# Kernel tuning notes

Hardware: AMD Instinct MI355X
Metric: run time of the kernel (lower is better)

Reference implementation:

```python
import jax, jax.numpy as jnp
import numpy as np

KH, KW = 3, 3
PAD = 1
IN_C = 3
OUT_C = 16
QUBITS = 5            # max(ceil(log2(3*3*3))=5, ceil(log2(16))=4)
QDEPTH = 1
DIM = 2 ** QUBITS     # 32 amplitudes per patch
FEAT = KH * KW * IN_C # 27 unfolded features per patch
EPS = 0.001           # self.almost_zero


def setup_inputs() -> dict:
    key = jax.random.key(0)
    k1, k2 = jax.random.split(key)
    x = jax.random.normal(k1, (8, 3, 224, 224), dtype=jnp.float32)
    # StronglyEntanglingLayer rotation angles (depth, qubits, 3) in [0, 2pi)
    weights = jax.random.uniform(k2, (QDEPTH, QUBITS, 3), dtype=jnp.float32,
                                 minval=0.0, maxval=2.0 * np.pi)
    return {"x": x, "weights": weights}


def _rot(phi, theta, omega):
    # PennyLane/qandle Rot(phi, theta, omega) = RZ(omega) RY(theta) RZ(phi)
    c = jnp.cos(theta * 0.5).astype(jnp.complex64)
    s = jnp.sin(theta * 0.5).astype(jnp.complex64)
    em = jnp.exp(-0.5j * (phi + omega))   # e^{-i(phi+omega)/2}
    ep = jnp.exp(0.5j * (phi + omega))
    epm = jnp.exp(0.5j * (phi - omega))
    emp = jnp.exp(-0.5j * (phi - omega))
    row0 = jnp.stack([em * c, -epm * s])
    row1 = jnp.stack([emp * s, ep * c])
    return jnp.stack([row0, row1])  # (2, 2) complex64


def _apply_1q(psi, U, q):
    # psi: (N, 2, 2, 2, 2, 2); apply 2x2 unitary on qubit q
    psi = jnp.moveaxis(psi, 1 + q, -1)
    psi = psi @ U.T  # new_a = sum_b U[a,b] psi[..., b]
    return jnp.moveaxis(psi, -1, 1 + q)


def _cnot(psi, c, t):
    # control qubit c, target qubit t: flip target where control == 1
    p0, p1 = jnp.split(psi, 2, axis=1 + c)
    p1 = jnp.flip(p1, axis=1 + t)
    return jnp.concatenate([p0, p1], axis=1 + c)


def reference(x, weights):
    b, cin, h, w = x.shape
    # --- Unfold (kernel 3x3, pad 1, stride 1) -> (b, c*kh*kw, h*w), torch layout ---
    xp = jnp.pad(x, ((0, 0), (0, 0), (PAD, PAD), (PAD, PAD)))
    cols = jnp.stack([xp[:, :, i:i + h, j:j + w]
                      for i in range(KH) for j in range(KW)], axis=2)  # (b, c, 9, h, w)
    v = cols.reshape(b, FEAT, h * w)
    # rearrange 'batch channel feat -> (batch feat) channel'
    v = jnp.transpose(v, (0, 2, 1)).reshape(b * h * w, FEAT) + EPS
    # --- AmplitudeEmbedding: pad with 0 to 2^qubits, L2-normalize ---
    v = jnp.pad(v, ((0, 0), (0, DIM - FEAT)))
    psi = (v / jnp.linalg.norm(v, axis=1, keepdims=True)).astype(jnp.complex64)
    psi = psi.reshape((b * h * w,) + (2,) * QUBITS)
    # --- StronglyEntanglingLayer: Rot on each qubit, then CNOT ring ---
    for d in range(QDEPTH):
        for q in range(QUBITS):
            U = _rot(weights[d, q, 0], weights[d, q, 1], weights[d, q, 2])
            psi = _apply_1q(psi, U, q)
        for q in range(QUBITS):
            psi = _cnot(psi, q, (q + 1) % QUBITS)
    # --- MeasureJointProbability: |amplitude|^2 over all basis states ---
    psi = psi.reshape(b * h * w, DIM)
    probs = psi.real ** 2 + psi.imag ** 2
    # --- post-process: keep first out_channels, scale ---
    out = probs[:, :OUT_C] * (OUT_C / 2.0)
    # rearrange '(batch h w) channel -> batch channel h w'
    out = jnp.transpose(out.reshape(b, h * w, OUT_C), (0, 2, 1))
    return out.reshape(b, OUT_C, h, w)
```

## Files before the change

### kernel.cpp

```cpp
#include <hip/hip_runtime.h>

#define H 224
#define W 224
#define NB 8
#define OUTC 16
#define FEAT 27
#define EPSV 0.001f

__global__ void build_M(const float* __restrict__ w, float2* __restrict__ M) {
    __shared__ float sre[32][33];
    __shared__ float sim_[32][33];
    const int j = threadIdx.x;

    for (int i = 0; i < 32; ++i) {
        sre[j][i] = (i == j) ? 1.0f : 0.0f;
        sim_[j][i] = 0.0f;
    }

    for (int q = 0; q < 5; ++q) {
        float phi = w[q * 3 + 0];
        float th  = w[q * 3 + 1];
        float om  = w[q * 3 + 2];
        float ch = cosf(0.5f * th), sh = sinf(0.5f * th);
        float al = 0.5f * (phi + om), be = 0.5f * (phi - om);
        float ca = cosf(al), sa = sinf(al);
        float cb = cosf(be), sb = sinf(be);
        float u00r =  ca * ch, u00i = -sa * ch;
        float u01r = -cb * sh, u01i = -sb * sh;
        float u10r =  cb * sh, u10i = -sb * sh;
        float u11r =  ca * ch, u11i =  sa * ch;

        int m = 1 << (4 - q);
        for (int i = 0; i < 32; ++i) {
            if (i & m) continue;
            float a0r = sre[j][i],     a0i = sim_[j][i];
            float a1r = sre[j][i | m], a1i = sim_[j][i | m];
            sre[j][i]     = u00r * a0r - u00i * a0i + u01r * a1r - u01i * a1i;
            sim_[j][i]    = u00r * a0i + u00i * a0r + u01r * a1i + u01i * a1r;
            sre[j][i | m] = u10r * a0r - u10i * a0i + u11r * a1r - u11i * a1i;
            sim_[j][i | m]= u10r * a0i + u10i * a0r + u11r * a1i + u11i * a1r;
        }
    }

    for (int q = 0; q < 5; ++q) {
        int mc = 1 << (4 - q);
        int mt = 1 << (4 - ((q + 1) % 5));
        for (int i = 0; i < 32; ++i) {
            if ((i & mc) && !(i & mt)) {
                int i2 = i | mt;
                float tr = sre[j][i]; sre[j][i] = sre[j][i2]; sre[j][i2] = tr;
                float ti = sim_[j][i]; sim_[j][i] = sim_[j][i2]; sim_[j][i2] = ti;
            }
        }
    }

    if (j < FEAT) {
        for (int k = 0; k < OUTC; ++k) {
            M[k * FEAT + j] = make_float2(sre[j][k], sim_[j][k]);
        }
    }
}

__global__ __launch_bounds__(256) void qconv_main(const float* __restrict__ x,
                                                  const float2* __restrict__ M,
                                                  float* __restrict__ out) {
    int p = blockIdx.x * 256 + threadIdx.x;
    int xx = p % W;
    int rest = p / W;
    int yy = rest % H;
    int b = rest / H;

    const float* xb = x + b * (3 * H * W);

    float v[FEAT];
    #pragma unroll
    for (int c = 0; c < 3; ++c) {
        #pragma unroll
        for (int ki = 0; ki < 3; ++ki) {
            #pragma unroll
            for (int kj = 0; kj < 3; ++kj) {
                int iy = yy + ki - 1;
                int ix = xx + kj - 1;
                float val = 0.0f;
                if (iy >= 0 && iy < H && ix >= 0 && ix < W)
                    val = xb[c * (H * W) + iy * W + ix];
                v[c * 9 + ki * 3 + kj] = val + EPSV;
            }
        }
    }

    float n2 = 0.0f;
    #pragma unroll
    for (int f = 0; f < FEAT; ++f) n2 = fmaf(v[f], v[f], n2);
    float scale = 8.0f / n2;

    float* ob = out + b * (OUTC * H * W) + yy * W + xx;
    #pragma unroll
    for (int k = 0; k < OUTC; ++k) {
        float re = 0.0f, im = 0.0f;
        #pragma unroll
        for (int f = 0; f < FEAT; ++f) {
            float2 m = M[k * FEAT + f];
            re = fmaf(m.x, v[f], re);
            im = fmaf(m.y, v[f], im);
        }
        ob[k * (H * W)] = (re * re + im * im) * scale;
    }
}

extern "C" void kernel_launch(void* const* d_in, const int* in_sizes, int n_in,
                              void* d_out, int out_size, void* d_ws, size_t ws_size,
                              hipStream_t stream) {
    const float* x = (const float*)d_in[0];
    const float* w = (const float*)d_in[1];
    float* out = (float*)d_out;
    float2* M = (float2*)d_ws;

    build_M<<<1, 32, 0, stream>>>(w, M);

    int pixels = out_size / OUTC;
    int blocks = (pixels + 255) / 256;
    qconv_main<<<blocks, 256, 0, stream>>>(x, M, out);
}
```

Baseline: 96.27 us.

## Pre-pad input with eps, compute 4 pixels per thread with vector loads

A prep kernel now writes a zero-padded, eps-added copy of the input into a workspace buffer, and the same launch builds the matrix M in its last block. The main kernel stages M in shared memory, and each thread handles 4 horizontally adjacent pixels and 8 of the 16 output channels. It loads 3x6 windows per channel with float4/float2 loads and stores outputs as float4. This is meant to cut redundant neighbourhood loads, remove bounds checks, and raise work per thread, at the cost of an extra full pass writing and reading a padded copy of the input.

```diff
diff --git a/kernel.cpp b/kernel.cpp
--- a/kernel.cpp
+++ b/kernel.cpp
@@ -2,109 +2,153 @@
 
 #define H 224
 #define W 224
-#define NB 8
+#define HW (H * W)
 #define OUTC 16
 #define FEAT 27
 #define EPSV 0.001f
+#define PH 226
+#define PW 228
+#define PLANE (PH * PW)
+#define NPAD (24 * PLANE)
+#define PAD_BLOCKS ((NPAD + 255) / 256)
 
-__global__ void build_M(const float* __restrict__ w, float2* __restrict__ M) {
-    __shared__ float sre[32][33];
-    __shared__ float sim_[32][33];
-    const int j = threadIdx.x;
+typedef float f4 __attribute__((ext_vector_type(4)));
+typedef float f2 __attribute__((ext_vector_type(2)));
 
-    for (int i = 0; i < 32; ++i) {
-        sre[j][i] = (i == j) ? 1.0f : 0.0f;
-        sim_[j][i] = 0.0f;
+__global__ __launch_bounds__(256) void prep(const float* __restrict__ x,
+                                            const float* __restrict__ w,
+                                            float* __restrict__ pbuf,
+                                            float2* __restrict__ M) {
+    if (blockIdx.x == gridDim.x - 1) {
+        __shared__ float sre[32][33];
+        __shared__ float sim_[32][33];
+        const int j = threadIdx.x;
+        if (j >= 32) return;
+
+        for (int i = 0; i < 32; ++i) {
+            sre[j][i] = (i == j) ? 1.0f : 0.0f;
+            sim_[j][i] = 0.0f;
+        }
+        for (int q = 0; q < 5; ++q) {
+            float phi = w[q * 3 + 0];
+            float th  = w[q * 3 + 1];
+            float om  = w[q * 3 + 2];
+            float ch = cosf(0.5f * th), sh = sinf(0.5f * th);
+            float al = 0.5f * (phi + om), be = 0.5f * (phi - om);
+            float ca = cosf(al), sa = sinf(al);
+            float cb = cosf(be), sb = sinf(be);
+            float u00r =  ca * ch, u00i = -sa * ch;
+            float u01r = -cb * sh, u01i = -sb * sh;
+            float u10r =  cb * sh, u10i = -sb * sh;
+            float u11r =  ca * ch, u11i =  sa * ch;
+            int m = 1 << (4 - q);
+            for (int i = 0; i < 32; ++i) {
+                if (i & m) continue;
+                float a0r = sre[j][i],     a0i = sim_[j][i];
+                float a1r = sre[j][i | m], a1i = sim_[j][i | m];
+                sre[j][i]      = u00r * a0r - u00i * a0i + u01r * a1r - u01i * a1i;
+                sim_[j][i]     = u00r * a0i + u00i * a0r + u01r * a1i + u01i * a1r;
+                sre[j][i | m]  = u10r * a0r - u10i * a0i + u11r * a1r - u11i * a1i;
+                sim_[j][i | m] = u10r * a0i + u10i * a0r + u11r * a1i + u11i * a1r;
+            }
+        }
+        for (int q = 0; q < 5; ++q) {
+            int mc = 1 << (4 - q);
+            int mt = 1 << (4 - ((q + 1) % 5));
+            for (int i = 0; i < 32; ++i) {
+                if ((i & mc) && !(i & mt)) {
+                    int i2 = i | mt;
+                    float tr = sre[j][i]; sre[j][i] = sre[j][i2]; sre[j][i2] = tr;
+                    float ti = sim_[j][i]; sim_[j][i] = sim_[j][i2]; sim_[j][i2] = ti;
+                }
+            }
+        }
+        if (j < FEAT) {
+            for (int k = 0; k < OUTC; ++k)
+                M[k * FEAT + j] = make_float2(sre[j][k], sim_[j][k]);
+        }
+        return;
     }
 
-    for (int q = 0; q < 5; ++q) {
-        float phi = w[q * 3 + 0];
-        float th  = w[q * 3 + 1];
-        float om  = w[q * 3 + 2];
-        float ch = cosf(0.5f * th), sh = sinf(0.5f * th);
-        float al = 0.5f * (phi + om), be = 0.5f * (phi - om);
-        float ca = cosf(al), sa = sinf(al);
-        float cb = cosf(be), sb = sinf(be);
-        float u00r =  ca * ch, u00i = -sa * ch;
-        float u01r = -cb * sh, u01i = -sb * sh;
-        float u10r =  cb * sh, u10i = -sb * sh;
-        float u11r =  ca * ch, u11i =  sa * ch;
-
-        int m = 1 << (4 - q);
-        for (int i = 0; i < 32; ++i) {
-            if (i & m) continue;
-            float a0r = sre[j][i],     a0i = sim_[j][i];
-            float a1r = sre[j][i | m], a1i = sim_[j][i | m];
-            sre[j][i]     = u00r * a0r - u00i * a0i + u01r * a1r - u01i * a1i;
-            sim_[j][i]    = u00r * a0i + u00i * a0r + u01r * a1i + u01i * a1r;
-            sre[j][i | m] = u10r * a0r - u10i * a0i + u11r * a1r - u11i * a1i;
-            sim_[j][i | m]= u10r * a0i + u10i * a0r + u11r * a1i + u11i * a1r;
-        }
-    }
-
-    for (int q = 0; q < 5; ++q) {
-        int mc = 1 << (4 - q);
-        int mt = 1 << (4 - ((q + 1) % 5));
-        for (int i = 0; i < 32; ++i) {
-            if ((i & mc) && !(i & mt)) {
-                int i2 = i | mt;
-                float tr = sre[j][i]; sre[j][i] = sre[j][i2]; sre[j][i2] = tr;
-                float ti = sim_[j][i]; sim_[j][i] = sim_[j][i2]; sim_[j][i2] = ti;
-            }
-        }
-    }
-
-    if (j < FEAT) {
-        for (int k = 0; k < OUTC; ++k) {
-            M[k * FEAT + j] = make_float2(sre[j][k], sim_[j][k]);
-        }
-    }
+    int i = blockIdx.x * 256 + threadIdx.x;
+    if (i >= NPAD) return;
+    int px = i % PW;
+    int rest = i / PW;
+    int py = rest % PH;
+    int cc = rest / PH;
+    float val = EPSV;
+    int ix = px - 1, iy = py - 1;
+    if (ix >= 0 && ix < W && iy >= 0 && iy < H)
+        val = x[cc * HW + iy * W + ix] + EPSV;
+    pbuf[i] = val;
 }
 
-__global__ __launch_bounds__(256) void qconv_main(const float* __restrict__ x,
-                                                  const float2* __restrict__ M,
-                                                  float* __restrict__ out) {
-    int p = blockIdx.x * 256 + threadIdx.x;
-    int xx = p % W;
-    int rest = p / W;
-    int yy = rest % H;
-    int b = rest / H;
+__global__ __launch_bounds__(256) void qconv(const float* __restrict__ pbuf,
+                                             const float2* __restrict__ M,
+                                             float* __restrict__ out) {
+    __shared__ float2 Ms[OUTC * FEAT];
+    const int tid = threadIdx.x;
+    Ms[tid] = M[tid];
+    if (tid < OUTC * FEAT - 256) Ms[256 + tid] = M[256 + tid];
+    __syncthreads();
 
-    const float* xb = x + b * (3 * H * W);
+    const int khalf = blockIdx.x & 1;
+    const int g = (blockIdx.x >> 1) * 256 + tid;
+    const int x4 = (g % 56) * 4;
+    int rest = g / 56;
+    const int y = rest % H;
+    const int b = rest / H;
 
-    float v[FEAT];
+    float r[3][3][6];
     #pragma unroll
     for (int c = 0; c < 3; ++c) {
         #pragma unroll
         for (int ki = 0; ki < 3; ++ki) {
-            #pragma unroll
-            for (int kj = 0; kj < 3; ++kj) {
-                int iy = yy + ki - 1;
-                int ix = xx + kj - 1;
-                float val = 0.0f;
-                if (iy >= 0 && iy < H && ix >= 0 && ix < W)
-                    val = xb[c * (H * W) + iy * W + ix];
-                v[c * 9 + ki * 3 + kj] = val + EPSV;
-            }
+            const float* rp = pbuf + ((b * 3 + c) * PLANE) + (y + ki) * PW + x4;
+            f4 a = *(const f4*)rp;
+            f2 t = *(const f2*)(rp + 4);
+            r[c][ki][0] = a.x; r[c][ki][1] = a.y; r[c][ki][2] = a.z; r[c][ki][3] = a.w;
+            r[c][ki][4] = t.x; r[c][ki][5] = t.y;
         }
     }
 
-    float n2 = 0.0f;
+    float scale[4];
     #pragma unroll
-    for (int f = 0; f < FEAT; ++f) n2 = fmaf(v[f], v[f], n2);
-    float scale = 8.0f / n2;
+    for (int p = 0; p < 4; ++p) {
+        float n2 = 0.0f;
+        #pragma unroll
+        for (int c = 0; c < 3; ++c)
+            #pragma unroll
+            for (int ki = 0; ki < 3; ++ki)
+                #pragma unroll
+                for (int kj = 0; kj < 3; ++kj) {
+                    float t = r[c][ki][p + kj];
+                    n2 = fmaf(t, t, n2);
+                }
+        scale[p] = 8.0f / n2;
+    }
 
-    float* ob = out + b * (OUTC * H * W) + yy * W + xx;
+    float* ob = out + ((size_t)b * OUTC + khalf * 8) * HW + y * W + x4;
     #pragma unroll
-    for (int k = 0; k < OUTC; ++k) {
-        float re = 0.0f, im = 0.0f;
+    for (int kk = 0; kk < 8; ++kk) {
+        float re[4] = {0, 0, 0, 0}, im[4] = {0, 0, 0, 0};
         #pragma unroll
         for (int f = 0; f < FEAT; ++f) {
-            float2 m = M[k * FEAT + f];
-            re = fmaf(m.x, v[f], re);
-            im = fmaf(m.y, v[f], im);
+            float2 m = Ms[(khalf * 8 + kk) * FEAT + f];
+            const int c = f / 9, rr = (f % 9) / 3, kj = f % 3;
+            #pragma unroll
+            for (int p = 0; p < 4; ++p) {
+                float t = r[c][rr][p + kj];
+                re[p] = fmaf(m.x, t, re[p]);
+                im[p] = fmaf(m.y, t, im[p]);
+            }
         }
-        ob[k * (H * W)] = (re * re + im * im) * scale;
+        f4 o;
+        o.x = (re[0] * re[0] + im[0] * im[0]) * scale[0];
+        o.y = (re[1] * re[1] + im[1] * im[1]) * scale[1];
+        o.z = (re[2] * re[2] + im[2] * im[2]) * scale[2];
+        o.w = (re[3] * re[3] + im[3] * im[3]) * scale[3];
+        *(f4*)(ob + kk * HW) = o;
     }
 }
 
@@ -114,11 +158,11 @@
     const float* x = (const float*)d_in[0];
     const float* w = (const float*)d_in[1];
     float* out = (float*)d_out;
+
     float2* M = (float2*)d_ws;
+    float* pbuf = (float*)((char*)d_ws + 4096);
 
-    build_M<<<1, 32, 0, stream>>>(w, M);
+    prep<<<PAD_BLOCKS + 1, 256, 0, stream>>>(x, w, pbuf, M);
 
-    int pixels = out_size / OUTC;
-    int blocks = (pixels + 255) / 256;
-    qconv_main<<<blocks, 256, 0, stream>>>(x, M, out);
+    qconv<<<784, 256, 0, stream>>>(pbuf, M, out);
 }
```

Measured after the change: 91.08 us. 1.06x faster.
